# Performance work log

Hardware: AMD Instinct MI355X
Metric: run time of the kernel (lower is better)

## Reference

```python
import jax, jax.numpy as jnp
import numpy as np

B, S, F, H = 2, 2048, 1024, 16
HD = F // H


def setup_inputs() -> dict:
    key = jax.random.key(0)
    ks = jax.random.split(key, 9)
    Q = jax.random.normal(ks[0], (B, S, F), dtype=jnp.float32)
    K = jax.random.normal(ks[1], (B, S, F), dtype=jnp.float32)
    V = jax.random.normal(ks[2], (B, S, F), dtype=jnp.float32)
    # additive pre-softmax causal mask: 0 on/below diagonal, -1e9 above
    causal = jnp.tril(jnp.ones((S, S), dtype=bool))
    mask_1 = jnp.where(causal, 0.0, -1e9).astype(jnp.float32)[None, None]
    # multiplicative post-softmax mask in [0,1)
    mask_2 = jax.random.uniform(ks[3], (1, 1, S, S), dtype=jnp.float32)
    scale = 1.0 / np.sqrt(F)
    W_q = jax.random.normal(ks[4], (F, F), dtype=jnp.float32) * scale
    W_k = jax.random.normal(ks[5], (F, F), dtype=jnp.float32) * scale
    W_v = jax.random.normal(ks[6], (F, F), dtype=jnp.float32) * scale
    W_o = jax.random.normal(ks[7], (F, F), dtype=jnp.float32) * scale
    return {"Q": Q, "K": K, "V": V, "mask_1": mask_1, "mask_2": mask_2,
            "W_q": W_q, "W_k": W_k, "W_v": W_v, "W_o": W_o}


def reference(Q, K, V, mask_1, mask_2, W_q, W_k, W_v, W_o):
    # Linear projections (no bias), split into heads: [B,S,F] -> [B,H,S,HD]
    def proj(x, W):
        return (x @ W.T).reshape(B, S, H, HD).transpose(0, 2, 1, 3)
    q, k, v = proj(Q, W_q), proj(K, W_k), proj(V, W_v)
    # scores [B,H,S,S], scaled by sqrt(head_size)
    scores = jnp.einsum('bhqd,bhkd->bhqk', q, k) / np.sqrt(HD)
    scores = scores + mask_1  # additive pre-softmax mask
    probs = jax.nn.softmax(scores, axis=-1) * mask_2  # multiplicative post-softmax mask
    out = jnp.einsum('bhqk,bhkd->bhqd', probs, v)
    out = out.transpose(0, 2, 1, 3).reshape(B, S, F)
    return out @ W_o.T
```

## Files before the change

### kernel.cpp

```cpp
#include <hip/hip_runtime.h>
#include <hip/hip_bf16.h>
#include <stdint.h>

typedef __bf16 bf16_t;
typedef __bf16 bf16x8 __attribute__((ext_vector_type(8)));
typedef __bf16 bf16x4v __attribute__((ext_vector_type(4)));
typedef float f32x4 __attribute__((ext_vector_type(4)));

#define GLDS16(g, l)                                                         \
  __builtin_amdgcn_global_load_lds(                                          \
      (const __attribute__((address_space(1))) void*)(g),                    \
      (__attribute__((address_space(3))) void*)(l), 16, 0, 0)

__device__ __forceinline__ f32x4 mfma16(bf16x8 a, bf16x8 b, f32x4 c) {
  return __builtin_amdgcn_mfma_f32_16x16x32_bf16(a, b, c, 0, 0, 0);
}

static constexpr int S = 2048, F = 1024, H = 16, HD = 64;

static constexpr size_t OFF_QB  = 0;
static constexpr size_t OFF_KB  = 4194304;
static constexpr size_t OFF_VB  = 8388608;
static constexpr size_t OFF_WQ  = 12582912;
static constexpr size_t OFF_WK  = 13631488;
static constexpr size_t OFF_WV  = 14680064;
static constexpr size_t OFF_WO  = 15728640;
static constexpr size_t OFF_QP  = 16777216;
static constexpr size_t OFF_KP  = 20971520;
static constexpr size_t OFF_VPT = 25165824;
static constexpr size_t OFF_M2  = 29360128;
static constexpr size_t OFF_ATT = 0;

__global__ void cvt_all(const float* __restrict__ s0, const float* __restrict__ s1,
                        const float* __restrict__ s2, const float* __restrict__ s3,
                        const float* __restrict__ w0, const float* __restrict__ w1,
                        const float* __restrict__ w2, const float* __restrict__ w3,
                        bf16_t* __restrict__ d0, bf16_t* __restrict__ d1,
                        bf16_t* __restrict__ d2, bf16_t* __restrict__ d3,
                        bf16_t* __restrict__ e0, bf16_t* __restrict__ e1,
                        bf16_t* __restrict__ e2, bf16_t* __restrict__ e3) {
  const float* s;
  bf16_t* d;
  size_t r;
  if (blockIdx.x < 8192) {
    int t = blockIdx.x * 256 + threadIdx.x;
    int a = t >> 19;
    r = (size_t)(t & 0x7FFFF) * 8;
    s = (a == 0) ? s0 : (a == 1) ? s1 : (a == 2) ? s2 : s3;
    d = (a == 0) ? d0 : (a == 1) ? d1 : (a == 2) ? d2 : d3;
  } else {
    int t = (blockIdx.x - 8192) * 256 + threadIdx.x;
    int a = t >> 17;
    r = (size_t)(t & 0x1FFFF) * 8;
    s = (a == 0) ? w0 : (a == 1) ? w1 : (a == 2) ? w2 : w3;
    d = (a == 0) ? e0 : (a == 1) ? e1 : (a == 2) ? e2 : e3;
  }
  const float4* sp = (const float4*)(s + r);
  float4 u = sp[0], v = sp[1];
  bf16x8 o;
  o[0] = (bf16_t)u.x; o[1] = (bf16_t)u.y; o[2] = (bf16_t)u.z; o[3] = (bf16_t)u.w;
  o[4] = (bf16_t)v.x; o[5] = (bf16_t)v.y; o[6] = (bf16_t)v.z; o[7] = (bf16_t)v.w;
  *(bf16x8*)(d + r) = o;
}

__device__ __forceinline__ void stage128x32(const bf16_t* __restrict__ g, int ld,
                                            bf16_t* lds, int wv, int ln) {
#pragma unroll
  for (int i = 0; i < 2; ++i) {
    int ch  = wv * 2 + i;
    int row = ch * 16 + (ln >> 2);
    int col = (ln & 3) * 8;
    GLDS16(g + (size_t)row * ld + col, lds + ch * 512);
  }
}

__global__ __launch_bounds__(256, 2) void proj_gemm(
    const bf16_t* __restrict__ Qb, const bf16_t* __restrict__ Kb, const bf16_t* __restrict__ Vb,
    const bf16_t* __restrict__ Wq, const bf16_t* __restrict__ Wk, const bf16_t* __restrict__ Wv,
    bf16_t* __restrict__ qp, bf16_t* __restrict__ kp, bf16_t* __restrict__ vpT) {
  __shared__ bf16_t As[2][128 * 32];
  __shared__ bf16_t Bs[2][128 * 32];
  const int z = blockIdx.z;
  const bf16_t* A = (z == 0) ? Qb : (z == 1) ? Kb : Vb;
  const bf16_t* W = (z == 0) ? Wq : (z == 1) ? Wk : Wv;
  const int m0 = blockIdx.x * 128, n0 = blockIdx.y * 128;
  const int tid = threadIdx.x, wv = tid >> 6, ln = tid & 63;
  const int wr = wv >> 1, wc = wv & 1, lr = ln & 15, lg = ln >> 4;
  f32x4 acc[4][4];
#pragma unroll
  for (int i = 0; i < 4; ++i)
#pragma unroll
    for (int j = 0; j < 4; ++j) acc[i][j] = (f32x4){0.f, 0.f, 0.f, 0.f};

  stage128x32(A + (size_t)m0 * F, F, As[0], wv, ln);
  stage128x32(W + (size_t)n0 * F, F, Bs[0], wv, ln);
  __syncthreads();

  for (int k0 = 0; k0 < F; k0 += 32) {
    const int cur = (k0 >> 5) & 1;
    if (k0 + 32 < F) {
      stage128x32(A + (size_t)m0 * F + k0 + 32, F, As[cur ^ 1], wv, ln);
      stage128x32(W + (size_t)n0 * F + k0 + 32, F, Bs[cur ^ 1], wv, ln);
    }
    bf16x8 af[4], bfr[4];
#pragma unroll
    for (int i = 0; i < 4; ++i)
      af[i] = *(const bf16x8*)&As[cur][(wr * 64 + i * 16 + lr) * 32 + lg * 8];
#pragma unroll
    for (int j = 0; j < 4; ++j)
      bfr[j] = *(const bf16x8*)&Bs[cur][(wc * 64 + j * 16 + lr) * 32 + lg * 8];
#pragma unroll
    for (int i = 0; i < 4; ++i)
#pragma unroll
      for (int j = 0; j < 4; ++j) acc[i][j] = mfma16(af[i], bfr[j], acc[i][j]);
    __syncthreads();
  }

  const int rbase = m0 + wr * 64, cbase = n0 + wc * 64;
  if (z < 2) {
    bf16_t* out = (z == 0) ? qp : kp;
    const float qscl = (z == 0) ? 0.18033688f : 1.0f;
#pragma unroll
    for (int i = 0; i < 4; ++i)
#pragma unroll
      for (int j = 0; j < 4; ++j) {
        int r0 = rbase + i * 16 + lg * 4;
        int c  = cbase + j * 16 + lr;
        int b = r0 >> 11, s = r0 & 2047, h = c >> 6, d = c & 63;
        size_t base = ((size_t)(b * H + h) * S + s) * HD + d;
#pragma unroll
        for (int reg = 0; reg < 4; ++reg)
          out[base + (size_t)reg * HD] = (bf16_t)(acc[i][j][reg] * qscl);
      }
  } else {
#pragma unroll
    for (int i = 0; i < 4; ++i)
#pragma unroll
      for (int j = 0; j < 4; ++j) {
        int r0 = rbase + i * 16 + lg * 4;
        int c  = cbase + j * 16 + lr;
        int b = r0 >> 11, s = r0 & 2047, h = c >> 6, d = c & 63;
        size_t base = ((size_t)(b * H + h) * HD + d) * S + s;
        bf16x4v pv;
#pragma unroll
        for (int reg = 0; reg < 4; ++reg) pv[reg] = (bf16_t)acc[i][j][reg];
        *(bf16x4v*)&vpT[base] = pv;
      }
  }
}

__global__ __launch_bounds__(256, 2) void out_gemm(
    const bf16_t* __restrict__ A, const bf16_t* __restrict__ W, float* __restrict__ out) {
  __shared__ bf16_t As[2][128 * 32];
  __shared__ bf16_t Bs[2][128 * 32];
  const int m0 = blockIdx.x * 128, n0 = blockIdx.y * 128;
  const int tid = threadIdx.x, wv = tid >> 6, ln = tid & 63;
  const int wr = wv >> 1, wc = wv & 1, lr = ln & 15, lg = ln >> 4;
  f32x4 acc[4][4];
#pragma unroll
  for (int i = 0; i < 4; ++i)
#pragma unroll
    for (int j = 0; j < 4; ++j) acc[i][j] = (f32x4){0.f, 0.f, 0.f, 0.f};

  stage128x32(A + (size_t)m0 * F, F, As[0], wv, ln);
  stage128x32(W + (size_t)n0 * F, F, Bs[0], wv, ln);
  __syncthreads();

  for (int k0 = 0; k0 < F; k0 += 32) {
    const int cur = (k0 >> 5) & 1;
    if (k0 + 32 < F) {
      stage128x32(A + (size_t)m0 * F + k0 + 32, F, As[cur ^ 1], wv, ln);
      stage128x32(W + (size_t)n0 * F + k0 + 32, F, Bs[cur ^ 1], wv, ln);
    }
    bf16x8 af[4], bfr[4];
#pragma unroll
    for (int i = 0; i < 4; ++i)
      af[i] = *(const bf16x8*)&As[cur][(wr * 64 + i * 16 + lr) * 32 + lg * 8];
#pragma unroll
    for (int j = 0; j < 4; ++j)
      bfr[j] = *(const bf16x8*)&Bs[cur][(wc * 64 + j * 16 + lr) * 32 + lg * 8];
#pragma unroll
    for (int i = 0; i < 4; ++i)
#pragma unroll
      for (int j = 0; j < 4; ++j) acc[i][j] = mfma16(af[i], bfr[j], acc[i][j]);
    __syncthreads();
  }
#pragma unroll
  for (int i = 0; i < 4; ++i)
#pragma unroll
    for (int j = 0; j < 4; ++j) {
      int r0 = m0 + wr * 64 + i * 16 + lg * 4;
      int c  = n0 + wc * 64 + j * 16 + lr;
#pragma unroll
      for (int reg = 0; reg < 4; ++reg)
        out[(size_t)(r0 + reg) * F + c] = acc[i][j][reg];
    }
}

__global__ __launch_bounds__(256, 4) void flash(
    const bf16_t* __restrict__ qp, const bf16_t* __restrict__ kp,
    const bf16_t* __restrict__ vpT, const bf16_t* __restrict__ m2b,
    bf16_t* __restrict__ PA, bf16_t* __restrict__ PB,
    float* __restrict__ lA, float* __restrict__ lB) {
  __shared__ bf16_t Ks[2][64 * 64];
  __shared__ bf16_t Vs[2][64 * 64];
  __shared__ bf16_t Pl[4][16 * 64];
  const int ur = blockIdx.x >> 5, bh = blockIdx.x & 31;
  const int grp = ur / 3, rem = ur % 3;
  int qt, kvlo, kvhi;
  if (rem == 2) { qt = 15 - grp; kvlo = 0; kvhi = qt; }
  else {
    qt = 31 - grp;
    int half = (qt + 2) >> 1;
    if (rem == 0) { kvlo = 0; kvhi = half - 1; }
    else          { kvlo = half; kvhi = qt; }
  }
  bf16_t* __restrict__ PO = (rem == 1) ? PB : PA;
  float*  __restrict__ LO = (rem == 1) ? lB : lA;

  const int tid = threadIdx.x, wv = tid >> 6, ln = tid & 63;
  const int lr = ln & 15, lg = ln >> 4;
  const bf16_t* qb = qp + (size_t)bh * S * HD;
  const bf16_t* kb = kp + (size_t)bh * S * HD;
  const bf16_t* vb = vpT + (size_t)bh * HD * S;
  const int q0w = qt * 64 + wv * 16;
  const int qg  = q0w + lr;

  bf16x8 bq[2];
#pragma unroll
  for (int h2 = 0; h2 < 2; ++h2)
    bq[h2] = *(const bf16x8*)&qb[(size_t)qg * HD + h2 * 32 + lg * 8];

  float ls = 0.f;
  f32x4 accv[4];
#pragma unroll
  for (int n = 0; n < 4; ++n) accv[n] = (f32x4){0.f, 0.f, 0.f, 0.f};

  const int srow0 = ln >> 3, scc0 = ln & 7;
  const int pxor = lr & 7;

#pragma unroll
  for (int i = 0; i < 2; ++i) {
    int ch = wv * 2 + i;
    int row = ch * 8 + srow0;
    int scc = scc0 ^ (row & 7);
    GLDS16(kb + (size_t)(kvlo * 64 + row) * HD + scc * 8, Ks[0] + ch * 512);
    GLDS16(vb + (size_t)row * S + kvlo * 64 + scc * 8, Vs[0] + ch * 512);
  }
  __syncthreads();

  for (int kt = kvlo; kt <= kvhi; ++kt) {
    const int k0 = kt * 64;
    const int cur = (kt - kvlo) & 1;

    bf16x4v m2v[4];
#pragma unroll
    for (int c = 0; c < 4; ++c)
      m2v[c] = *(const bf16x4v*)&m2b[(size_t)qg * S + k0 + c * 16 + lg * 4];

    if (kt < kvhi) {
      const int kn = k0 + 64;
#pragma unroll
      for (int i = 0; i < 2; ++i) {
        int ch = wv * 2 + i;
        int row = ch * 8 + srow0;
        int scc = scc0 ^ (row & 7);
        GLDS16(kb + (size_t)(kn + row) * HD + scc * 8, Ks[cur ^ 1] + ch * 512);
        GLDS16(vb + (size_t)row * S + kn + scc * 8, Vs[cur ^ 1] + ch * 512);
      }
    }

    f32x4 st[4];
    __builtin_amdgcn_s_setprio(1);
#pragma unroll
    for (int c = 0; c < 4; ++c) {
      int kr = c * 16 + lr;
      int sw = kr & 7;
      bf16x8 ak0 = *(const bf16x8*)&Ks[cur][kr * 64 + ((lg ^ sw) * 8)];
      bf16x8 ak1 = *(const bf16x8*)&Ks[cur][kr * 64 + (((4 + lg) ^ sw) * 8)];
      f32x4 t = (f32x4){0.f, 0.f, 0.f, 0.f};
      t = mfma16(ak0, bq[0], t);
      t = mfma16(ak1, bq[1], t);
      st[c] = t;
    }
    __builtin_amdgcn_s_setprio(0);
    if (kt == qt) {
#pragma unroll
      for (int c = 0; c < 4; ++c)
#pragma unroll
        for (int r = 0; r < 4; ++r) {
          int kgl = k0 + c * 16 + lg * 4 + r;
          if (kgl > qg) st[c][r] = -1e30f;
        }
    }
#pragma unroll
    for (int c = 0; c < 4; ++c) {
      bf16x4v pw;
      float p0 = exp2f(st[c][0]), p1 = exp2f(st[c][1]);
      float p2 = exp2f(st[c][2]), p3 = exp2f(st[c][3]);
      ls += (p0 + p1) + (p2 + p3);
      pw[0] = (bf16_t)(p0 * (float)m2v[c][0]);
      pw[1] = (bf16_t)(p1 * (float)m2v[c][1]);
      pw[2] = (bf16_t)(p2 * (float)m2v[c][2]);
      pw[3] = (bf16_t)(p3 * (float)m2v[c][3]);
      int chunk = (2 * c + (lg >> 1)) ^ pxor;
      *(bf16x4v*)&Pl[wv][lr * 64 + chunk * 8 + (lg & 1) * 4] = pw;
    }
    __builtin_amdgcn_s_setprio(1);
#pragma unroll
    for (int kc = 0; kc < 2; ++kc) {
      int pchunk = (4 * kc + lg) ^ pxor;
      bf16x8 pb = *(const bf16x8*)&Pl[wv][lr * 64 + pchunk * 8];
#pragma unroll
      for (int n = 0; n < 4; ++n) {
        int dr = n * 16 + lr;
        int sw = dr & 7;
        bf16x8 av = *(const bf16x8*)&Vs[cur][dr * 64 + (((kc * 4 + lg) ^ sw) * 8)];
        accv[n] = mfma16(av, pb, accv[n]);
      }
    }
    __builtin_amdgcn_s_setprio(0);
    __syncthreads();
  }

  ls += __shfl_xor(ls, 16, 64);
  ls += __shfl_xor(ls, 32, 64);
  if (lg == 0) LO[bh * S + qg] = ls;
#pragma unroll
  for (int n = 0; n < 4; ++n) {
    bf16x4v ov;
#pragma unroll
    for (int r = 0; r < 4; ++r) ov[r] = (bf16_t)accv[n][r];
    *(bf16x4v*)&PO[((size_t)bh * S + qg) * HD + n * 16 + lg * 4] = ov;
  }
}

__global__ void norm_cvt(const bf16_t* __restrict__ PA, const bf16_t* __restrict__ PB,
                         const float* __restrict__ lA, const float* __restrict__ lB,
                         bf16_t* __restrict__ att) {
  int t = blockIdx.x * 256 + threadIdx.x;
  int bh = t >> 13;
  int rm = t & 8191;
  int s  = rm >> 2;
  int d0 = (rm & 3) * 16;
  size_t pbase = ((size_t)bh * S + s) * HD + d0;
  bf16x8 a0 = *(const bf16x8*)&PA[pbase];
  bf16x8 a1 = *(const bf16x8*)&PA[pbase + 8];
  float l = lA[bh * S + s];
  float o[16];
#pragma unroll
  for (int i = 0; i < 8; ++i) { o[i] = (float)a0[i]; o[8 + i] = (float)a1[i]; }
  if (s >= 1024) {
    bf16x8 b0 = *(const bf16x8*)&PB[pbase];
    bf16x8 b1 = *(const bf16x8*)&PB[pbase + 8];
    l += lB[bh * S + s];
#pragma unroll
    for (int i = 0; i < 8; ++i) { o[i] += (float)b0[i]; o[8 + i] += (float)b1[i]; }
  }
  float inv = 1.0f / l;
  int b = bh >> 4, h = bh & 15;
  bf16x8 w0, w1;
#pragma unroll
  for (int i = 0; i < 8; ++i) {
    w0[i] = (bf16_t)(o[i] * inv);
    w1[i] = (bf16_t)(o[8 + i] * inv);
  }
  size_t obase = ((size_t)(b * S + s)) * F + h * HD + d0;
  *(bf16x8*)&att[obase] = w0;
  *(bf16x8*)&att[obase + 8] = w1;
}

extern "C" void kernel_launch(void* const* d_in, const int* in_sizes, int n_in,
                              void* d_out, int out_size, void* d_ws, size_t ws_size,
                              hipStream_t stream) {
  (void)in_sizes; (void)n_in; (void)out_size; (void)ws_size;
  const float* Q  = (const float*)d_in[0];
  const float* K  = (const float*)d_in[1];
  const float* V  = (const float*)d_in[2];
  const float* M2 = (const float*)d_in[4];
  const float* Wq = (const float*)d_in[5];
  const float* Wk = (const float*)d_in[6];
  const float* Wv = (const float*)d_in[7];
  const float* Wo = (const float*)d_in[8];
  bf16_t* ws = (bf16_t*)d_ws;

  bf16_t *Qb = ws + OFF_QB, *Kb = ws + OFF_KB, *Vb = ws + OFF_VB;
  bf16_t *WqB = ws + OFF_WQ, *WkB = ws + OFF_WK, *WvB = ws + OFF_WV, *WoB = ws + OFF_WO;
  bf16_t *qpB = ws + OFF_QP, *kpB = ws + OFF_KP, *vpT = ws + OFF_VPT;
  bf16_t *m2b = ws + OFF_M2, *att = ws + OFF_ATT;
  bf16_t *PA = ws + OFF_KB, *PB = ws + OFF_VB;
  float  *lA = (float*)(ws + OFF_WQ), *lB = (float*)(ws + OFF_WK);

  cvt_all<<<10240, 256, 0, stream>>>(Q, K, V, M2, Wq, Wk, Wv, Wo,
                                     Qb, Kb, Vb, m2b, WqB, WkB, WvB, WoB);
  proj_gemm<<<dim3(32, 8, 3), 256, 0, stream>>>(Qb, Kb, Vb, WqB, WkB, WvB, qpB, kpB, vpT);
  flash<<<dim3(1536), 256, 0, stream>>>(qpB, kpB, vpT, m2b, PA, PB, lA, lB);
  norm_cvt<<<1024, 256, 0, stream>>>(PA, PB, lA, lB, att);
  out_gemm<<<dim3(32, 8), 256, 0, stream>>>(att, WoB, (float*)d_out);
}
```

Measured before the change: 137.3 us.

## Fuse input fp32->bf16 conversion into projection GEMM and normalization into output GEMM

The projection GEMM now reads fp32 Q/K/V directly, converting to bf16 in registers and writing the results into LDS. This removes the separate conversion pass over the activations and its bf16 round trip through memory. The output GEMM now reads the flash partials PA/PB and row sums lA/lB, merges and normalizes them while staging the A tile, and the standalone norm_cvt kernel is dropped. The trade-offs are that A-tile loads become synchronous register loads instead of async global-to-LDS copies, fp32 A loads are twice as wide, and the A staging path gains extra ALU work and branching.

```diff
diff --git a/kernel.cpp b/kernel.cpp
--- a/kernel.cpp
+++ b/kernel.cpp
@@ -18,9 +18,8 @@
 
 static constexpr int S = 2048, F = 1024, H = 16, HD = 64;
 
-static constexpr size_t OFF_QB  = 0;
-static constexpr size_t OFF_KB  = 4194304;
-static constexpr size_t OFF_VB  = 8388608;
+static constexpr size_t OFF_PA  = 4194304;
+static constexpr size_t OFF_PB  = 8388608;
 static constexpr size_t OFF_WQ  = 12582912;
 static constexpr size_t OFF_WK  = 13631488;
 static constexpr size_t OFF_WV  = 14680064;
@@ -29,27 +28,21 @@
 static constexpr size_t OFF_KP  = 20971520;
 static constexpr size_t OFF_VPT = 25165824;
 static constexpr size_t OFF_M2  = 29360128;
-static constexpr size_t OFF_ATT = 0;
-
-__global__ void cvt_all(const float* __restrict__ s0, const float* __restrict__ s1,
-                        const float* __restrict__ s2, const float* __restrict__ s3,
-                        const float* __restrict__ w0, const float* __restrict__ w1,
-                        const float* __restrict__ w2, const float* __restrict__ w3,
-                        bf16_t* __restrict__ d0, bf16_t* __restrict__ d1,
-                        bf16_t* __restrict__ d2, bf16_t* __restrict__ d3,
-                        bf16_t* __restrict__ e0, bf16_t* __restrict__ e1,
-                        bf16_t* __restrict__ e2, bf16_t* __restrict__ e3) {
+
+__global__ void cvt_small(const float* __restrict__ m2, const float* __restrict__ w0,
+                          const float* __restrict__ w1, const float* __restrict__ w2,
+                          const float* __restrict__ w3, bf16_t* __restrict__ dm,
+                          bf16_t* __restrict__ e0, bf16_t* __restrict__ e1,
+                          bf16_t* __restrict__ e2, bf16_t* __restrict__ e3) {
   const float* s;
   bf16_t* d;
   size_t r;
-  if (blockIdx.x < 8192) {
+  if (blockIdx.x < 2048) {
     int t = blockIdx.x * 256 + threadIdx.x;
-    int a = t >> 19;
-    r = (size_t)(t & 0x7FFFF) * 8;
-    s = (a == 0) ? s0 : (a == 1) ? s1 : (a == 2) ? s2 : s3;
-    d = (a == 0) ? d0 : (a == 1) ? d1 : (a == 2) ? d2 : d3;
+    r = (size_t)t * 8;
+    s = m2; d = dm;
   } else {
-    int t = (blockIdx.x - 8192) * 256 + threadIdx.x;
+    int t = (blockIdx.x - 2048) * 256 + threadIdx.x;
     int a = t >> 17;
     r = (size_t)(t & 0x1FFFF) * 8;
     s = (a == 0) ? w0 : (a == 1) ? w1 : (a == 2) ? w2 : w3;
@@ -74,32 +67,58 @@
   }
 }
 
+__device__ __forceinline__ void pack16(const float4& p0, const float4& p1,
+                                       const float4& p2, const float4& p3,
+                                       float qscl, bf16x8& w0, bf16x8& w1) {
+  w0[0] = (bf16_t)(p0.x * qscl); w0[1] = (bf16_t)(p0.y * qscl);
+  w0[2] = (bf16_t)(p0.z * qscl); w0[3] = (bf16_t)(p0.w * qscl);
+  w0[4] = (bf16_t)(p1.x * qscl); w0[5] = (bf16_t)(p1.y * qscl);
+  w0[6] = (bf16_t)(p1.z * qscl); w0[7] = (bf16_t)(p1.w * qscl);
+  w1[0] = (bf16_t)(p2.x * qscl); w1[1] = (bf16_t)(p2.y * qscl);
+  w1[2] = (bf16_t)(p2.z * qscl); w1[3] = (bf16_t)(p2.w * qscl);
+  w1[4] = (bf16_t)(p3.x * qscl); w1[5] = (bf16_t)(p3.y * qscl);
+  w1[6] = (bf16_t)(p3.z * qscl); w1[7] = (bf16_t)(p3.w * qscl);
+}
+
 __global__ __launch_bounds__(256, 2) void proj_gemm(
-    const bf16_t* __restrict__ Qb, const bf16_t* __restrict__ Kb, const bf16_t* __restrict__ Vb,
+    const float* __restrict__ Qf, const float* __restrict__ Kf, const float* __restrict__ Vf,
     const bf16_t* __restrict__ Wq, const bf16_t* __restrict__ Wk, const bf16_t* __restrict__ Wv,
     bf16_t* __restrict__ qp, bf16_t* __restrict__ kp, bf16_t* __restrict__ vpT) {
   __shared__ bf16_t As[2][128 * 32];
   __shared__ bf16_t Bs[2][128 * 32];
   const int z = blockIdx.z;
-  const bf16_t* A = (z == 0) ? Qb : (z == 1) ? Kb : Vb;
+  const float* A = (z == 0) ? Qf : (z == 1) ? Kf : Vf;
   const bf16_t* W = (z == 0) ? Wq : (z == 1) ? Wk : Wv;
   const int m0 = blockIdx.x * 128, n0 = blockIdx.y * 128;
   const int tid = threadIdx.x, wv = tid >> 6, ln = tid & 63;
   const int wr = wv >> 1, wc = wv & 1, lr = ln & 15, lg = ln >> 4;
+  const int ar = tid >> 1, ac = (tid & 1) * 16;
+  const float* ag = A + (size_t)(m0 + ar) * F + ac;
   f32x4 acc[4][4];
 #pragma unroll
   for (int i = 0; i < 4; ++i)
 #pragma unroll
     for (int j = 0; j < 4; ++j) acc[i][j] = (f32x4){0.f, 0.f, 0.f, 0.f};
 
-  stage128x32(A + (size_t)m0 * F, F, As[0], wv, ln);
-  stage128x32(W + (size_t)n0 * F, F, Bs[0], wv, ln);
+  {
+    float4 p0 = *(const float4*)(ag + 0), p1 = *(const float4*)(ag + 4);
+    float4 p2 = *(const float4*)(ag + 8), p3 = *(const float4*)(ag + 12);
+    stage128x32(W + (size_t)n0 * F, F, Bs[0], wv, ln);
+    bf16x8 w0, w1;
+    pack16(p0, p1, p2, p3, 1.0f, w0, w1);
+    *(bf16x8*)&As[0][ar * 32 + ac] = w0;
+    *(bf16x8*)&As[0][ar * 32 + ac + 8] = w1;
+  }
   __syncthreads();
 
   for (int k0 = 0; k0 < F; k0 += 32) {
     const int cur = (k0 >> 5) & 1;
-    if (k0 + 32 < F) {
-      stage128x32(A + (size_t)m0 * F + k0 + 32, F, As[cur ^ 1], wv, ln);
+    const bool pre = (k0 + 32 < F);
+    float4 p0, p1, p2, p3;
+    if (pre) {
+      const float* an = ag + k0 + 32;
+      p0 = *(const float4*)(an + 0); p1 = *(const float4*)(an + 4);
+      p2 = *(const float4*)(an + 8); p3 = *(const float4*)(an + 12);
       stage128x32(W + (size_t)n0 * F + k0 + 32, F, Bs[cur ^ 1], wv, ln);
     }
     bf16x8 af[4], bfr[4];
@@ -113,6 +132,12 @@
     for (int i = 0; i < 4; ++i)
 #pragma unroll
       for (int j = 0; j < 4; ++j) acc[i][j] = mfma16(af[i], bfr[j], acc[i][j]);
+    if (pre) {
+      bf16x8 w0, w1;
+      pack16(p0, p1, p2, p3, 1.0f, w0, w1);
+      *(bf16x8*)&As[cur ^ 1][ar * 32 + ac] = w0;
+      *(bf16x8*)&As[cur ^ 1][ar * 32 + ac + 8] = w1;
+    }
     __syncthreads();
   }
 
@@ -150,27 +175,68 @@
 }
 
 __global__ __launch_bounds__(256, 2) void out_gemm(
-    const bf16_t* __restrict__ A, const bf16_t* __restrict__ W, float* __restrict__ out) {
+    const bf16_t* __restrict__ PA, const bf16_t* __restrict__ PB,
+    const float* __restrict__ lA, const float* __restrict__ lB,
+    const bf16_t* __restrict__ W, float* __restrict__ out) {
   __shared__ bf16_t As[2][128 * 32];
   __shared__ bf16_t Bs[2][128 * 32];
   const int m0 = blockIdx.x * 128, n0 = blockIdx.y * 128;
   const int tid = threadIdx.x, wv = tid >> 6, ln = tid & 63;
   const int wr = wv >> 1, wc = wv & 1, lr = ln & 15, lg = ln >> 4;
+  const int ar = tid >> 1, ac = (tid & 1) * 16;
+  const int row = m0 + ar, s = row & 2047, b = row >> 11;
+  const bool hiS = (s >= 1024);
   f32x4 acc[4][4];
 #pragma unroll
   for (int i = 0; i < 4; ++i)
 #pragma unroll
     for (int j = 0; j < 4; ++j) acc[i][j] = (f32x4){0.f, 0.f, 0.f, 0.f};
 
-  stage128x32(A + (size_t)m0 * F, F, As[0], wv, ln);
-  stage128x32(W + (size_t)n0 * F, F, Bs[0], wv, ln);
+  {
+    size_t pb0 = ((size_t)(b * 16) * S + s) * HD + ac;
+    bf16x8 a0 = *(const bf16x8*)&PA[pb0];
+    bf16x8 a1 = *(const bf16x8*)&PA[pb0 + 8];
+    float lv = lA[(b * 16) * S + s], lw = 0.f;
+    float va[16];
+#pragma unroll
+    for (int e = 0; e < 8; ++e) { va[e] = (float)a0[e]; va[8 + e] = (float)a1[e]; }
+    if (hiS) {
+      bf16x8 b0 = *(const bf16x8*)&PB[pb0];
+      bf16x8 b1 = *(const bf16x8*)&PB[pb0 + 8];
+      lw = lB[(b * 16) * S + s];
+#pragma unroll
+      for (int e = 0; e < 8; ++e) { va[e] += (float)b0[e]; va[8 + e] += (float)b1[e]; }
+    }
+    stage128x32(W + (size_t)n0 * F, F, Bs[0], wv, ln);
+    float inv = 1.0f / (lv + lw);
+    bf16x8 w0, w1;
+#pragma unroll
+    for (int e = 0; e < 8; ++e) {
+      w0[e] = (bf16_t)(va[e] * inv);
+      w1[e] = (bf16_t)(va[8 + e] * inv);
+    }
+    *(bf16x8*)&As[0][ar * 32 + ac] = w0;
+    *(bf16x8*)&As[0][ar * 32 + ac + 8] = w1;
+  }
   __syncthreads();
 
   for (int k0 = 0; k0 < F; k0 += 32) {
     const int cur = (k0 >> 5) & 1;
-    if (k0 + 32 < F) {
-      stage128x32(A + (size_t)m0 * F + k0 + 32, F, As[cur ^ 1], wv, ln);
-      stage128x32(W + (size_t)n0 * F + k0 + 32, F, Bs[cur ^ 1], wv, ln);
+    const bool pre = (k0 + 32 < F);
+    bf16x8 a0, a1, pb0v, pb1v;
+    float lv = 0.f, lw = 0.f;
+    if (pre) {
+      const int kn = k0 + 32, h = kn >> 6, d0 = (kn & 63) + ac;
+      size_t pbase = ((size_t)(b * 16 + h) * S + s) * HD + d0;
+      a0 = *(const bf16x8*)&PA[pbase];
+      a1 = *(const bf16x8*)&PA[pbase + 8];
+      lv = lA[(b * 16 + h) * S + s];
+      if (hiS) {
+        pb0v = *(const bf16x8*)&PB[pbase];
+        pb1v = *(const bf16x8*)&PB[pbase + 8];
+        lw = lB[(b * 16 + h) * S + s];
+      }
+      stage128x32(W + (size_t)n0 * F + kn, F, Bs[cur ^ 1], wv, ln);
     }
     bf16x8 af[4], bfr[4];
 #pragma unroll
@@ -183,6 +249,24 @@
     for (int i = 0; i < 4; ++i)
 #pragma unroll
       for (int j = 0; j < 4; ++j) acc[i][j] = mfma16(af[i], bfr[j], acc[i][j]);
+    if (pre) {
+      float va[16];
+#pragma unroll
+      for (int e = 0; e < 8; ++e) { va[e] = (float)a0[e]; va[8 + e] = (float)a1[e]; }
+      if (hiS) {
+#pragma unroll
+        for (int e = 0; e < 8; ++e) { va[e] += (float)pb0v[e]; va[8 + e] += (float)pb1v[e]; }
+      }
+      float inv = 1.0f / (lv + lw);
+      bf16x8 w0, w1;
+#pragma unroll
+      for (int e = 0; e < 8; ++e) {
+        w0[e] = (bf16_t)(va[e] * inv);
+        w1[e] = (bf16_t)(va[8 + e] * inv);
+      }
+      *(bf16x8*)&As[cur ^ 1][ar * 32 + ac] = w0;
+      *(bf16x8*)&As[cur ^ 1][ar * 32 + ac + 8] = w1;
+    }
     __syncthreads();
   }
 #pragma unroll
@@ -335,41 +419,6 @@
   }
 }
 
-__global__ void norm_cvt(const bf16_t* __restrict__ PA, const bf16_t* __restrict__ PB,
-                         const float* __restrict__ lA, const float* __restrict__ lB,
-                         bf16_t* __restrict__ att) {
-  int t = blockIdx.x * 256 + threadIdx.x;
-  int bh = t >> 13;
-  int rm = t & 8191;
-  int s  = rm >> 2;
-  int d0 = (rm & 3) * 16;
-  size_t pbase = ((size_t)bh * S + s) * HD + d0;
-  bf16x8 a0 = *(const bf16x8*)&PA[pbase];
-  bf16x8 a1 = *(const bf16x8*)&PA[pbase + 8];
-  float l = lA[bh * S + s];
-  float o[16];
-#pragma unroll
-  for (int i = 0; i < 8; ++i) { o[i] = (float)a0[i]; o[8 + i] = (float)a1[i]; }
-  if (s >= 1024) {
-    bf16x8 b0 = *(const bf16x8*)&PB[pbase];
-    bf16x8 b1 = *(const bf16x8*)&PB[pbase + 8];
-    l += lB[bh * S + s];
-#pragma unroll
-    for (int i = 0; i < 8; ++i) { o[i] += (float)b0[i]; o[8 + i] += (float)b1[i]; }
-  }
-  float inv = 1.0f / l;
-  int b = bh >> 4, h = bh & 15;
-  bf16x8 w0, w1;
-#pragma unroll
-  for (int i = 0; i < 8; ++i) {
-    w0[i] = (bf16_t)(o[i] * inv);
-    w1[i] = (bf16_t)(o[8 + i] * inv);
-  }
-  size_t obase = ((size_t)(b * S + s)) * F + h * HD + d0;
-  *(bf16x8*)&att[obase] = w0;
-  *(bf16x8*)&att[obase + 8] = w1;
-}
-
 extern "C" void kernel_launch(void* const* d_in, const int* in_sizes, int n_in,
                               void* d_out, int out_size, void* d_ws, size_t ws_size,
                               hipStream_t stream) {
@@ -384,17 +433,14 @@
   const float* Wo = (const float*)d_in[8];
   bf16_t* ws = (bf16_t*)d_ws;
 
-  bf16_t *Qb = ws + OFF_QB, *Kb = ws + OFF_KB, *Vb = ws + OFF_VB;
   bf16_t *WqB = ws + OFF_WQ, *WkB = ws + OFF_WK, *WvB = ws + OFF_WV, *WoB = ws + OFF_WO;
   bf16_t *qpB = ws + OFF_QP, *kpB = ws + OFF_KP, *vpT = ws + OFF_VPT;
-  bf16_t *m2b = ws + OFF_M2, *att = ws + OFF_ATT;
-  bf16_t *PA = ws + OFF_KB, *PB = ws + OFF_VB;
+  bf16_t *m2b = ws + OFF_M2;
+  bf16_t *PA = ws + OFF_PA, *PB = ws + OFF_PB;
   float  *lA = (float*)(ws + OFF_WQ), *lB = (float*)(ws + OFF_WK);
 
-  cvt_all<<<10240, 256, 0, stream>>>(Q, K, V, M2, Wq, Wk, Wv, Wo,
-                                     Qb, Kb, Vb, m2b, WqB, WkB, WvB, WoB);
-  proj_gemm<<<dim3(32, 8, 3), 256, 0, stream>>>(Qb, Kb, Vb, WqB, WkB, WvB, qpB, kpB, vpT);
+  cvt_small<<<4096, 256, 0, stream>>>(M2, Wq, Wk, Wv, Wo, m2b, WqB, WkB, WvB, WoB);
+  proj_gemm<<<dim3(32, 8, 3), 256, 0, stream>>>(Q, K, V, WqB, WkB, WvB, qpB, kpB, vpT);
   flash<<<dim3(1536), 256, 0, stream>>>(qpB, kpB, vpT, m2b, PA, PB, lA, lB);
-  norm_cvt<<<1024, 256, 0, stream>>>(PA, PB, lA, lB, att);
-  out_gemm<<<dim3(32, 8), 256, 0, stream>>>(att, WoB, (float*)d_out);
-}
+  out_gemm<<<dim3(32, 8), 256, 0, stream>>>(PA, PB, lA, lB, WoB, (float*)d_out);
+}
```

New measurement: 158.3 us. 1.15x slower.
